# Performance work log

Measured on AMD Instinct MI355X. Metric: run time of the kernel, lower is better.

The kernel has to match this reference:

```python
import jax, jax.numpy as jnp
import numpy as np

B, K, D, H = 8192, 64, 384, 64
TOPK = min(8, K)


def setup_inputs() -> dict:
    key = jax.random.key(0)
    ks = jax.random.split(key, 9)
    F_in = 2 * D + 3
    return {
        "M": jax.random.normal(ks[0], (B, K, D), dtype=jnp.float32),
        "y": jax.random.uniform(ks[1], (B, K), dtype=jnp.float32),
        "timestamps": jax.random.uniform(ks[2], (B, K), dtype=jnp.float32),
        "W1": jax.random.normal(ks[3], (F_in, H), dtype=jnp.float32) / np.sqrt(F_in),
        "b1": jnp.zeros((H,), dtype=jnp.float32),
        "W2": jax.random.normal(ks[4], (H, H // 2), dtype=jnp.float32) / np.sqrt(H),
        "b2": jnp.zeros((H // 2,), dtype=jnp.float32),
        "W3": jax.random.normal(ks[5], (H // 2, 1), dtype=jnp.float32) / np.sqrt(H // 2),
        "b3": jnp.zeros((1,), dtype=jnp.float32),
    }


def reference(M, y, timestamps, W1, b1, W2, b2, W3, b3):
    # top-k selection (indices are constants wrt grad; values gathered below)
    _, idx = jax.lax.top_k(y, TOPK)                               # [B, TOPK]
    m_top = jnp.take_along_axis(M, idx[..., None], axis=1)        # [B, TOPK, D]
    t_top = jnp.take_along_axis(timestamps, idx, axis=1)          # [B, TOPK]
    y_top = jnp.take_along_axis(y, idx, axis=1)                   # [B, TOPK]

    # all 28 ordered pairs i<j, vectorized (replaces the python double loop)
    ii, jj = np.triu_indices(TOPK, k=1)                           # each [P]
    m_i, m_j = m_top[:, ii], m_top[:, jj]                         # [B, P, D]
    dt = (t_top[:, ii] - t_top[:, jj])[..., None]                 # [B, P, 1] signed
    y_i, y_j = y_top[:, ii], y_top[:, jj]                         # [B, P]
    pair = jnp.concatenate([m_i, m_j, dt, y_i[..., None], y_j[..., None]], axis=-1)  # [B, P, 2D+3]

    h = jax.nn.silu(pair @ W1 + b1)
    h = jax.nn.silu(h @ W2 + b2)
    penalty = (h @ W3 + b3)[..., 0]                               # [B, P]
    return jnp.sum(penalty * (y_i * y_j), axis=1)                 # [B]
```

## Files before the change

### kernel.cpp

```cpp
#include <hip/hip_runtime.h>

#define KC    64
#define DD    384
#define HH    64
#define H2    32
#define NTOP  8
#define NPAIR 28

#define NEG_INF (-3.402823466e38f)

__constant__ int c_ii[NPAIR] = {0,0,0,0,0,0,0, 1,1,1,1,1,1, 2,2,2,2,2, 3,3,3,3, 4,4,4, 5,5, 6};
__constant__ int c_jj[NPAIR] = {1,2,3,4,5,6,7, 2,3,4,5,6,7, 3,4,5,6,7, 4,5,6,7, 5,6,7, 6,7, 7};

__device__ __forceinline__ float silu_f(float x) {
    return x / (1.0f + __expf(-x));
}

__launch_bounds__(256, 4)
__global__ void rpe_kernel(const float* __restrict__ M,
                           const float* __restrict__ y,
                           const float* __restrict__ ts,
                           const float* __restrict__ W1,
                           const float* __restrict__ b1,
                           const float* __restrict__ W2,
                           const float* __restrict__ b2,
                           const float* __restrict__ W3,
                           const float* __restrict__ b3,
                           float* __restrict__ out)
{
    const int b   = blockIdx.x;
    const int tid = threadIdx.x;

    __shared__ int   s_idx[NTOP];
    __shared__ float s_ytop[NTOP];
    __shared__ float s_t[NTOP];
    __shared__ __align__(16) float s_buf[4 * NTOP * 128];
    __shared__ __align__(16) float s_P[NTOP * 128];
    __shared__ __align__(16) float s_h1[NPAIR * HH];
    __shared__ float s_pen[NPAIR];

    if (tid < 64) {
        float v = y[(size_t)b * KC + tid];
        #pragma unroll
        for (int r = 0; r < NTOP; ++r) {
            float bv = v; int bi = tid;
            #pragma unroll
            for (int off = 32; off >= 1; off >>= 1) {
                float ov = __shfl_xor(bv, off, 64);
                int   oi = __shfl_xor(bi, off, 64);
                if (ov > bv || (ov == bv && oi < bi)) { bv = ov; bi = oi; }
            }
            if (tid == 0) { s_idx[r] = bi; s_ytop[r] = bv; }
            if (tid == bi) v = NEG_INF;
        }
        if (tid < NTOP) {
            s_t[tid] = ts[(size_t)b * KC + s_idx[tid]];
        }
    }
    __syncthreads();

    float* s_m = s_buf;
    for (int q = tid; q < NTOP * 96; q += 256) {
        int r = q / 96, c4 = q - r * 96;
        const float4 v4 = *(const float4*)(M + ((size_t)b * KC + s_idx[r]) * DD + c4 * 4);
        *(float4*)(s_m + r * DD + c4 * 4) = v4;
    }
    __syncthreads();

    {
        const int g  = tid >> 5;
        const int lg = tid & 31;
        const int n0 = lg * 4;
        const float* wp = (n0 < HH) ? (W1 + n0) : (W1 + DD * HH + (n0 - HH));
        float acc[NTOP][4];
        #pragma unroll
        for (int k = 0; k < NTOP; ++k) {
            acc[k][0] = 0.f; acc[k][1] = 0.f; acc[k][2] = 0.f; acc[k][3] = 0.f;
        }
        const int d0 = g * 48;
        #pragma unroll 4
        for (int dd = 0; dd < 48; ++dd) {
            const int d = d0 + dd;
            const float4 w = *(const float4*)(wp + (size_t)d * HH);
            #pragma unroll
            for (int k = 0; k < NTOP; ++k) {
                const float mv = s_m[k * DD + d];
                acc[k][0] = fmaf(mv, w.x, acc[k][0]);
                acc[k][1] = fmaf(mv, w.y, acc[k][1]);
                acc[k][2] = fmaf(mv, w.z, acc[k][2]);
                acc[k][3] = fmaf(mv, w.w, acc[k][3]);
            }
        }
        #pragma unroll
        for (int k = 0; k < NTOP; ++k) {
            #pragma unroll
            for (int j = 0; j < 4; ++j)
                acc[k][j] += __shfl_xor(acc[k][j], 32, 64);
        }
        __syncthreads();
        const int w = tid >> 6;
        if ((tid & 63) < 32) {
            #pragma unroll
            for (int k = 0; k < NTOP; ++k) {
                #pragma unroll
                for (int j = 0; j < 4; ++j)
                    s_buf[w * 1024 + k * 128 + n0 + j] = acc[k][j];
            }
        }
    }
    __syncthreads();
    for (int q = tid; q < NTOP * 128; q += 256) {
        s_P[q] = s_buf[q] + s_buf[1024 + q] + s_buf[2048 + q] + s_buf[3072 + q];
    }
    __syncthreads();

    for (int q = tid; q < NPAIR * HH; q += 256) {
        const int p = q >> 6;
        const int n = q & 63;
        const int i = c_ii[p], j = c_jj[p];
        float x = s_P[i * 128 + n] + s_P[j * 128 + 64 + n]
                + (s_t[i] - s_t[j]) * W1[768 * HH + n]
                + s_ytop[i]         * W1[769 * HH + n]
                + s_ytop[j]         * W1[770 * HH + n]
                + b1[n];
        s_h1[q] = silu_f(x);
    }
    __syncthreads();

    if (tid < NPAIR * 8) {
        const int p  = tid >> 3;
        const int s  = tid & 7;
        const int m0 = s * 4;
        float a0 = 0.f, a1 = 0.f, a2 = 0.f, a3 = 0.f;
        #pragma unroll 8
        for (int d2 = 0; d2 < HH; ++d2) {
            const float hv = s_h1[p * HH + d2];
            const float4 w2 = *(const float4*)(W2 + d2 * H2 + m0);
            a0 = fmaf(hv, w2.x, a0);
            a1 = fmaf(hv, w2.y, a1);
            a2 = fmaf(hv, w2.z, a2);
            a3 = fmaf(hv, w2.w, a3);
        }
        float pe = silu_f(a0 + b2[m0 + 0]) * W3[m0 + 0]
                 + silu_f(a1 + b2[m0 + 1]) * W3[m0 + 1]
                 + silu_f(a2 + b2[m0 + 2]) * W3[m0 + 2]
                 + silu_f(a3 + b2[m0 + 3]) * W3[m0 + 3];
        #pragma unroll
        for (int off = 4; off >= 1; off >>= 1)
            pe += __shfl_down(pe, off, 8);
        if (s == 0) {
            const int i = c_ii[p], j = c_jj[p];
            s_pen[p] = (pe + b3[0]) * (s_ytop[i] * s_ytop[j]);
        }
    }
    __syncthreads();

    if (tid == 0) {
        float sum = 0.f;
        for (int p = 0; p < NPAIR; ++p) sum += s_pen[p];
        out[b] = sum;
    }
}

extern "C" void kernel_launch(void* const* d_in, const int* in_sizes, int n_in,
                              void* d_out, int out_size, void* d_ws, size_t ws_size,
                              hipStream_t stream) {
    const float* M  = (const float*)d_in[0];
    const float* y  = (const float*)d_in[1];
    const float* ts = (const float*)d_in[2];
    const float* W1 = (const float*)d_in[3];
    const float* b1 = (const float*)d_in[4];
    const float* W2 = (const float*)d_in[5];
    const float* b2 = (const float*)d_in[6];
    const float* W3 = (const float*)d_in[7];
    const float* b3 = (const float*)d_in[8];
    float* out = (float*)d_out;

    const int B = in_sizes[1] / KC;
    rpe_kernel<<<dim3(B), dim3(256), 0, stream>>>(M, y, ts, W1, b1, W2, b2, W3, b3, out);
}
```

Measured before the change: 1.026 ms.

## Use bf16 MFMA for first layer, process two batch rows per block

Adds a prep kernel that converts W1's two 384-row halves to bf16 in MFMA fragment layout, and replaces the scalar FP32 first-layer GEMM with 16x16x32 bf16 MFMA over 16 gathered rows (two batches per block). W2 and the small bias/weight vectors are staged into LDS, and the top-k, gather and MLP stages are split across two batch elements per block. This is meant to cut FP32 FMA cost and per-block overhead, at the price of bf16 rounding of M and W1 and an extra launch.

```diff
diff --git a/kernel.cpp b/kernel.cpp
--- a/kernel.cpp
+++ b/kernel.cpp
@@ -6,8 +6,12 @@
 #define H2    32
 #define NTOP  8
 #define NPAIR 28
+#define NKB   12
 
 #define NEG_INF (-3.402823466e38f)
+
+typedef __attribute__((ext_vector_type(8))) short short8;
+typedef __attribute__((ext_vector_type(4))) float floatx4;
 
 __constant__ int c_ii[NPAIR] = {0,0,0,0,0,0,0, 1,1,1,1,1,1, 2,2,2,2,2, 3,3,3,3, 4,4,4, 5,5, 6};
 __constant__ int c_jj[NPAIR] = {1,2,3,4,5,6,7, 2,3,4,5,6,7, 3,4,5,6,7, 4,5,6,7, 5,6,7, 6,7, 7};
@@ -15,6 +19,39 @@
 __device__ __forceinline__ float silu_f(float x) {
     return x / (1.0f + __expf(-x));
 }
+
+__device__ __forceinline__ unsigned short f2bf(float f) {
+    unsigned int u = __float_as_uint(f);
+    u += 0x7FFFu + ((u >> 16) & 1u);
+    return (unsigned short)(u >> 16);
+}
+
+__global__ void prep_w1(const float* __restrict__ W1, unsigned short* __restrict__ wf) {
+    const int blk  = blockIdx.x;
+    const int t    = blk / NKB;
+    const int kb   = blk - t * NKB;
+    const int lane = threadIdx.x;
+    const int quad = lane >> 4;
+    const int col  = lane & 15;
+    const int n    = t * 16 + col;
+    const int base_k = kb * 32 + quad * 8;
+    const int row_off = (n < HH) ? 0 : 384;
+    const int c       = (n < HH) ? n : n - HH;
+    unsigned short us[8];
+    #pragma unroll
+    for (int j = 0; j < 8; ++j) {
+        us[j] = f2bf(W1[(size_t)(row_off + base_k + j) * HH + c]);
+    }
+    short8 v;
+    #pragma unroll
+    for (int j = 0; j < 8; ++j) v[j] = (short)us[j];
+    *(short8*)(wf + ((size_t)(t * NKB + kb) * 64 + lane) * 8) = v;
+}
+
+union ABUnion {
+    short a[NKB * 64 * 8];
+    float h1[2 * NPAIR * HH];
+};
 
 __launch_bounds__(256, 4)
 __global__ void rpe_kernel(const float* __restrict__ M,
@@ -26,139 +63,171 @@
                            const float* __restrict__ b2,
                            const float* __restrict__ W3,
                            const float* __restrict__ b3,
+                           const unsigned short* __restrict__ wf,
                            float* __restrict__ out)
 {
-    const int b   = blockIdx.x;
+    const int blk = blockIdx.x;
     const int tid = threadIdx.x;
 
-    __shared__ int   s_idx[NTOP];
-    __shared__ float s_ytop[NTOP];
-    __shared__ float s_t[NTOP];
-    __shared__ __align__(16) float s_buf[4 * NTOP * 128];
-    __shared__ __align__(16) float s_P[NTOP * 128];
-    __shared__ __align__(16) float s_h1[NPAIR * HH];
-    __shared__ float s_pen[NPAIR];
-
-    if (tid < 64) {
-        float v = y[(size_t)b * KC + tid];
+    __shared__ __align__(16) ABUnion s_u;
+    __shared__ __align__(16) float s_P[16 * 128];
+    __shared__ __align__(16) float s_W2[HH * H2];
+    __shared__ float s_misc[324];
+    __shared__ int   s_idx[2][NTOP];
+    __shared__ float s_ytop[2][NTOP];
+    __shared__ float s_t[2][NTOP];
+    __shared__ float s_pen[2 * NPAIR];
+
+    if (tid < 128) {
+        const int w    = tid >> 6;
+        const int lane = tid & 63;
+        const size_t bb = (size_t)blk * 2 + w;
+        float v = y[bb * KC + lane];
+        float myv = 0.f; int myi = 0;
         #pragma unroll
         for (int r = 0; r < NTOP; ++r) {
-            float bv = v; int bi = tid;
+            float bv = v; int bi = lane;
             #pragma unroll
             for (int off = 32; off >= 1; off >>= 1) {
                 float ov = __shfl_xor(bv, off, 64);
                 int   oi = __shfl_xor(bi, off, 64);
                 if (ov > bv || (ov == bv && oi < bi)) { bv = ov; bi = oi; }
             }
-            if (tid == 0) { s_idx[r] = bi; s_ytop[r] = bv; }
-            if (tid == bi) v = NEG_INF;
-        }
-        if (tid < NTOP) {
-            s_t[tid] = ts[(size_t)b * KC + s_idx[tid]];
-        }
-    }
-    __syncthreads();
-
-    float* s_m = s_buf;
-    for (int q = tid; q < NTOP * 96; q += 256) {
-        int r = q / 96, c4 = q - r * 96;
-        const float4 v4 = *(const float4*)(M + ((size_t)b * KC + s_idx[r]) * DD + c4 * 4);
-        *(float4*)(s_m + r * DD + c4 * 4) = v4;
+            if (lane == r) { myv = bv; myi = bi; }
+            if (lane == bi) v = NEG_INF;
+        }
+        if (lane < NTOP) {
+            s_idx[w][lane]  = myi;
+            s_ytop[w][lane] = myv;
+            s_t[w][lane]    = ts[bb * KC + myi];
+        }
+    } else {
+        const int lt = tid - 128;
+        for (int q = lt; q < (HH * H2) / 4; q += 128)
+            ((float4*)s_W2)[q] = ((const float4*)W2)[q];
+        if (lt < 64) {
+            s_misc[lt]       = W1[(size_t)768 * HH + lt];
+            s_misc[64 + lt]  = W1[(size_t)769 * HH + lt];
+            s_misc[128 + lt] = W1[(size_t)770 * HH + lt];
+            s_misc[192 + lt] = b1[lt];
+        } else if (lt < 96) {
+            const int z = lt - 64;
+            s_misc[256 + z] = b2[z];
+            s_misc[288 + z] = W3[z];
+        } else if (lt == 96) {
+            s_misc[320] = b3[0];
+        }
+    }
+    __syncthreads();
+
+    for (int q = tid; q < 16 * 48; q += 256) {
+        const int m  = q / 48;
+        const int k8 = q - m * 48;
+        const int row = s_idx[m >> 3][m & 7];
+        const size_t bb = (size_t)blk * 2 + (m >> 3);
+        const float* src = M + ((bb * KC + row) * DD) + k8 * 8;
+        const float4 f0 = *(const float4*)(src);
+        const float4 f1 = *(const float4*)(src + 4);
+        short8 v;
+        v[0] = (short)f2bf(f0.x); v[1] = (short)f2bf(f0.y);
+        v[2] = (short)f2bf(f0.z); v[3] = (short)f2bf(f0.w);
+        v[4] = (short)f2bf(f1.x); v[5] = (short)f2bf(f1.y);
+        v[6] = (short)f2bf(f1.z); v[7] = (short)f2bf(f1.w);
+        const int kb = k8 >> 2, quad = k8 & 3;
+        *(short8*)(&s_u.a[((kb * 64) + quad * 16 + m) * 8]) = v;
     }
     __syncthreads();
 
     {
-        const int g  = tid >> 5;
-        const int lg = tid & 31;
-        const int n0 = lg * 4;
-        const float* wp = (n0 < HH) ? (W1 + n0) : (W1 + DD * HH + (n0 - HH));
-        float acc[NTOP][4];
-        #pragma unroll
-        for (int k = 0; k < NTOP; ++k) {
-            acc[k][0] = 0.f; acc[k][1] = 0.f; acc[k][2] = 0.f; acc[k][3] = 0.f;
-        }
-        const int d0 = g * 48;
+        const int w    = tid >> 6;
+        const int lane = tid & 63;
+        const int t0 = 2 * w, t1 = 2 * w + 1;
+        floatx4 acc0 = {0.f, 0.f, 0.f, 0.f};
+        floatx4 acc1 = {0.f, 0.f, 0.f, 0.f};
+        const short8* bf0 = (const short8*)(wf + ((size_t)t0 * NKB * 64) * 8);
+        const short8* bf1 = (const short8*)(wf + ((size_t)t1 * NKB * 64) * 8);
         #pragma unroll 4
-        for (int dd = 0; dd < 48; ++dd) {
-            const int d = d0 + dd;
-            const float4 w = *(const float4*)(wp + (size_t)d * HH);
+        for (int kb = 0; kb < NKB; ++kb) {
+            const short8 a  = *(const short8*)(&s_u.a[(kb * 64 + lane) * 8]);
+            const short8 bx = bf0[kb * 64 + lane];
+            const short8 by = bf1[kb * 64 + lane];
+            acc0 = __builtin_amdgcn_mfma_f32_16x16x32_bf16(a, bx, acc0, 0, 0, 0);
+            acc1 = __builtin_amdgcn_mfma_f32_16x16x32_bf16(a, by, acc1, 0, 0, 0);
+        }
+        const int col = lane & 15, quad = lane >> 4;
+        #pragma unroll
+        for (int r = 0; r < 4; ++r) {
+            const int row = quad * 4 + r;
+            s_P[row * 128 + t0 * 16 + col] = acc0[r];
+            s_P[row * 128 + t1 * 16 + col] = acc1[r];
+        }
+    }
+    __syncthreads();
+
+    {
+        const int hb = tid >> 7;
+        const int lt = tid & 127;
+        for (int q = lt; q < NPAIR * HH; q += 128) {
+            const int p = q >> 6;
+            const int n = q & 63;
+            const int i = c_ii[p], j = c_jj[p];
+            float x = s_P[(hb * 8 + i) * 128 + n]
+                    + s_P[(hb * 8 + j) * 128 + 64 + n]
+                    + (s_t[hb][i] - s_t[hb][j]) * s_misc[n]
+                    + s_ytop[hb][i]             * s_misc[64 + n]
+                    + s_ytop[hb][j]             * s_misc[128 + n]
+                    + s_misc[192 + n];
+            s_u.h1[(hb * NPAIR + p) * HH + n] = silu_f(x);
+        }
+    }
+    __syncthreads();
+
+    {
+        const int hb = tid >> 7;
+        const int lt = tid & 127;
+        if (lt < NPAIR * 4) {
+            const int p  = lt >> 2;
+            const int s  = lt & 3;
+            const int m0 = s * 8;
+            float acc[8];
             #pragma unroll
-            for (int k = 0; k < NTOP; ++k) {
-                const float mv = s_m[k * DD + d];
-                acc[k][0] = fmaf(mv, w.x, acc[k][0]);
-                acc[k][1] = fmaf(mv, w.y, acc[k][1]);
-                acc[k][2] = fmaf(mv, w.z, acc[k][2]);
-                acc[k][3] = fmaf(mv, w.w, acc[k][3]);
+            for (int c = 0; c < 8; ++c) acc[c] = 0.f;
+            const float* h1p = &s_u.h1[(hb * NPAIR + p) * HH];
+            #pragma unroll 8
+            for (int d2 = 0; d2 < HH; ++d2) {
+                const float hv = h1p[d2];
+                const float4 wlo = *(const float4*)(&s_W2[d2 * H2 + m0]);
+                const float4 whi = *(const float4*)(&s_W2[d2 * H2 + m0 + 4]);
+                acc[0] = fmaf(hv, wlo.x, acc[0]); acc[1] = fmaf(hv, wlo.y, acc[1]);
+                acc[2] = fmaf(hv, wlo.z, acc[2]); acc[3] = fmaf(hv, wlo.w, acc[3]);
+                acc[4] = fmaf(hv, whi.x, acc[4]); acc[5] = fmaf(hv, whi.y, acc[5]);
+                acc[6] = fmaf(hv, whi.z, acc[6]); acc[7] = fmaf(hv, whi.w, acc[7]);
             }
-        }
-        #pragma unroll
-        for (int k = 0; k < NTOP; ++k) {
+            float pe = 0.f;
             #pragma unroll
-            for (int j = 0; j < 4; ++j)
-                acc[k][j] += __shfl_xor(acc[k][j], 32, 64);
-        }
-        __syncthreads();
-        const int w = tid >> 6;
-        if ((tid & 63) < 32) {
-            #pragma unroll
-            for (int k = 0; k < NTOP; ++k) {
-                #pragma unroll
-                for (int j = 0; j < 4; ++j)
-                    s_buf[w * 1024 + k * 128 + n0 + j] = acc[k][j];
+            for (int c = 0; c < 8; ++c)
+                pe += silu_f(acc[c] + s_misc[256 + m0 + c]) * s_misc[288 + m0 + c];
+            pe += __shfl_down(pe, 2, 4);
+            pe += __shfl_down(pe, 1, 4);
+            if (s == 0) {
+                const int i = c_ii[p], j = c_jj[p];
+                s_pen[hb * NPAIR + p] = (pe + s_misc[320]) * (s_ytop[hb][i] * s_ytop[hb][j]);
             }
-        }
-    }
-    __syncthreads();
-    for (int q = tid; q < NTOP * 128; q += 256) {
-        s_P[q] = s_buf[q] + s_buf[1024 + q] + s_buf[2048 + q] + s_buf[3072 + q];
-    }
-    __syncthreads();
-
-    for (int q = tid; q < NPAIR * HH; q += 256) {
-        const int p = q >> 6;
-        const int n = q & 63;
-        const int i = c_ii[p], j = c_jj[p];
-        float x = s_P[i * 128 + n] + s_P[j * 128 + 64 + n]
-                + (s_t[i] - s_t[j]) * W1[768 * HH + n]
-                + s_ytop[i]         * W1[769 * HH + n]
-                + s_ytop[j]         * W1[770 * HH + n]
-                + b1[n];
-        s_h1[q] = silu_f(x);
-    }
-    __syncthreads();
-
-    if (tid < NPAIR * 8) {
-        const int p  = tid >> 3;
-        const int s  = tid & 7;
-        const int m0 = s * 4;
-        float a0 = 0.f, a1 = 0.f, a2 = 0.f, a3 = 0.f;
-        #pragma unroll 8
-        for (int d2 = 0; d2 < HH; ++d2) {
-            const float hv = s_h1[p * HH + d2];
-            const float4 w2 = *(const float4*)(W2 + d2 * H2 + m0);
-            a0 = fmaf(hv, w2.x, a0);
-            a1 = fmaf(hv, w2.y, a1);
-            a2 = fmaf(hv, w2.z, a2);
-            a3 = fmaf(hv, w2.w, a3);
-        }
-        float pe = silu_f(a0 + b2[m0 + 0]) * W3[m0 + 0]
-                 + silu_f(a1 + b2[m0 + 1]) * W3[m0 + 1]
-                 + silu_f(a2 + b2[m0 + 2]) * W3[m0 + 2]
-                 + silu_f(a3 + b2[m0 + 3]) * W3[m0 + 3];
-        #pragma unroll
-        for (int off = 4; off >= 1; off >>= 1)
-            pe += __shfl_down(pe, off, 8);
-        if (s == 0) {
-            const int i = c_ii[p], j = c_jj[p];
-            s_pen[p] = (pe + b3[0]) * (s_ytop[i] * s_ytop[j]);
         }
     }
     __syncthreads();
 
     if (tid == 0) {
         float sum = 0.f;
+        #pragma unroll
         for (int p = 0; p < NPAIR; ++p) sum += s_pen[p];
-        out[b] = sum;
+        out[(size_t)blk * 2] = sum;
+    }
+    if (tid == 128) {
+        float sum = 0.f;
+        #pragma unroll
+        for (int p = 0; p < NPAIR; ++p) sum += s_pen[NPAIR + p];
+        out[(size_t)blk * 2 + 1] = sum;
     }
 }
 
@@ -175,7 +244,10 @@
     const float* W3 = (const float*)d_in[7];
     const float* b3 = (const float*)d_in[8];
     float* out = (float*)d_out;
+    unsigned short* wf = (unsigned short*)d_ws;
 
     const int B = in_sizes[1] / KC;
-    rpe_kernel<<<dim3(B), dim3(256), 0, stream>>>(M, y, ts, W1, b1, W2, b2, W3, b3, out);
-}
+
+    prep_w1<<<dim3(8 * NKB), dim3(64), 0, stream>>>(W1, wf);
+    rpe_kernel<<<dim3(B / 2), dim3(256), 0, stream>>>(M, y, ts, W1, b1, W2, b2, W3, b3, wf, out);
+}
```

After: 939.6 us. 8.4% less time.
